# Kernel tuning notes

Hardware: AMD Instinct MI355X
Metric: run time of the kernel (lower is better)

## Reference

```python
import jax, jax.numpy as jnp
import numpy as np

N = 100000
E = 1600000
NFEAT = 128
NHID = 16
HEADS = 4
NCLASS = 40
NEG_SLOPE = 0.2
BN_EPS = 1e-5


def setup_inputs() -> dict:
    key = jax.random.key(0)
    ks = jax.random.split(key, 16)
    HC = NHID * HEADS  # 64
    x = jax.random.normal(ks[0], (N, NFEAT), dtype=jnp.float32)
    edge_index = jax.random.randint(ks[1], (2, E), 0, N, dtype=jnp.int64)
    def glorot(k, shape, fan_in):
        return jax.random.normal(k, shape, dtype=jnp.float32) * (1.0 / np.sqrt(fan_in))
    return {
        "x": x,
        "edge_index": edge_index,
        # layer 1: GATConv(NFEAT -> NHID, heads=HEADS, concat=True)
        "W1": glorot(ks[2], (NFEAT, HC), NFEAT),
        "att_src1": glorot(ks[3], (HEADS, NHID), NHID),
        "att_dst1": glorot(ks[4], (HEADS, NHID), NHID),
        "bias1": jnp.zeros((HC,), dtype=jnp.float32),
        # BatchNorm1d(HC), eval mode (running stats)
        "bn_gamma": jnp.ones((HC,), dtype=jnp.float32),
        "bn_beta": jnp.zeros((HC,), dtype=jnp.float32),
        "bn_mean": jax.random.normal(ks[5], (HC,), dtype=jnp.float32) * 0.1,
        "bn_var": jax.random.uniform(ks[6], (HC,), dtype=jnp.float32, minval=0.5, maxval=1.5),
        # layer 2: GATConv(HC -> NCLASS, heads=1, concat=False)
        "W2": glorot(ks[7], (HC, NCLASS), HC),
        "att_src2": glorot(ks[8], (1, NCLASS), NCLASS),
        "att_dst2": glorot(ks[9], (1, NCLASS), NCLASS),
        "bias2": jnp.zeros((NCLASS,), dtype=jnp.float32),
    }


def gat_conv(x, src, dst, W, att_src, att_dst, bias, concat):
    """PyG GATConv (eval; self-loops assumed already appended to src/dst)."""
    H, C = att_src.shape
    n = x.shape[0]
    h = (x @ W).reshape(n, H, C)                         # [N,H,C]
    a_s = (h * att_src[None]).sum(-1)                    # [N,H]
    a_d = (h * att_dst[None]).sum(-1)                    # [N,H]
    alpha = jax.nn.leaky_relu(a_s[src] + a_d[dst], NEG_SLOPE)  # [Et,H]
    # segment softmax over incoming edges of each destination node
    amax = jax.ops.segment_max(alpha, dst, num_segments=n)    # [N,H]
    ex = jnp.exp(alpha - amax[dst])
    denom = jax.ops.segment_sum(ex, dst, num_segments=n)
    coef = ex / denom[dst]                               # [Et,H]
    msg = h[src] * coef[:, :, None]                      # [Et,H,C]
    out = jax.ops.segment_sum(msg, dst, num_segments=n)  # [N,H,C]
    out = out.reshape(n, H * C) if concat else out.mean(axis=1)
    return out + bias


def reference(x, edge_index, W1, att_src1, att_dst1, bias1,
              bn_gamma, bn_beta, bn_mean, bn_var,
              W2, att_src2, att_dst2, bias2):
    n = x.shape[0]
    loops = jnp.arange(n, dtype=edge_index.dtype)
    src = jnp.concatenate([edge_index[0], loops])
    dst = jnp.concatenate([edge_index[1], loops])
    h = gat_conv(x, src, dst, W1, att_src1, att_dst1, bias1, concat=True)
    h = (h - bn_mean) * jax.lax.rsqrt(bn_var + BN_EPS) * bn_gamma + bn_beta
    h = jax.nn.relu(h)  # dropout is identity in eval
    out = gat_conv(h, src, dst, W2, att_src2, att_dst2, bias2, concat=False)
    return out
```

## Files before the change

### kernel.cpp

```cpp
#include <hip/hip_runtime.h>
#include <hip/hip_bf16.h>
#include <hip/hip_fp16.h>

#define NFEAT  128
#define HC     64
#define HEADS  4
#define NHID   16
#define NCLASS 40
#define NEG    0.2f
#define BN_EPS 1e-5f

#define BK_SH   9
#define CHUNK   8192
#define STAGE   12288

typedef _Float16 half8_t __attribute__((ext_vector_type(8)));
typedef _Float16 half4_t __attribute__((ext_vector_type(4)));
typedef float    f32x4_t __attribute__((ext_vector_type(4)));

__device__ __forceinline__ float leaky(float a) { return (a > 0.f) ? a : NEG * a; }

__global__ __launch_bounds__(256) void k_gemm1(
    const float* __restrict__ x, const float* __restrict__ W1,
    const float* __restrict__ att_s, const float* __restrict__ att_d,
    __half* __restrict__ h1, float* __restrict__ as1, float* __restrict__ ad1,
    int n)
{
    const int wave = threadIdx.x >> 6, lane = threadIdx.x & 63;
    const int quad = lane >> 4, l16 = lane & 15;

    half8_t bfrag[4][4];
    #pragma unroll
    for (int ks = 0; ks < 4; ++ks)
        #pragma unroll
        for (int ct = 0; ct < 4; ++ct)
            #pragma unroll
            for (int j = 0; j < 8; ++j)
                bfrag[ks][ct][j] =
                    (_Float16)W1[(ks * 32 + quad * 8 + j) * HC + ct * 16 + l16];

    float avs[4], avd[4];
    #pragma unroll
    for (int ct = 0; ct < 4; ++ct) {
        avs[ct] = att_s[ct * 16 + l16];
        avd[ct] = att_d[ct * 16 + l16];
    }

    const int nslab = (n + 15) >> 4;
    for (int slab = blockIdx.x * 4 + wave; slab < nslab; slab += gridDim.x * 4) {
        const int rowbase = slab * 16;
        const int arow = min(rowbase + l16, n - 1);
        const float* xp = x + (size_t)arow * NFEAT;

        f32x4_t acc[4] = {{0.f,0.f,0.f,0.f},{0.f,0.f,0.f,0.f},
                          {0.f,0.f,0.f,0.f},{0.f,0.f,0.f,0.f}};
        #pragma unroll
        for (int ks = 0; ks < 4; ++ks) {
            const float4 xa = *(const float4*)(xp + ks * 32 + quad * 8);
            const float4 xb = *(const float4*)(xp + ks * 32 + quad * 8 + 4);
            half8_t af;
            af[0] = (_Float16)xa.x; af[1] = (_Float16)xa.y;
            af[2] = (_Float16)xa.z; af[3] = (_Float16)xa.w;
            af[4] = (_Float16)xb.x; af[5] = (_Float16)xb.y;
            af[6] = (_Float16)xb.z; af[7] = (_Float16)xb.w;
            #pragma unroll
            for (int ct = 0; ct < 4; ++ct)
                acc[ct] = __builtin_amdgcn_mfma_f32_16x16x32_f16(
                    af, bfrag[ks][ct], acc[ct], 0, 0, 0);
        }

        #pragma unroll
        for (int reg = 0; reg < 4; ++reg) {
            const int row = rowbase + quad * 4 + reg;
            const bool valid = row < n;

            float4 ps, pd;
            ps.x = acc[0][reg] * avs[0]; pd.x = acc[0][reg] * avd[0];
            ps.y = acc[1][reg] * avs[1]; pd.y = acc[1][reg] * avd[1];
            ps.z = acc[2][reg] * avs[2]; pd.z = acc[2][reg] * avd[2];
            ps.w = acc[3][reg] * avs[3]; pd.w = acc[3][reg] * avd[3];
            #pragma unroll
            for (int off = 8; off >= 1; off >>= 1) {
                ps.x += __shfl_xor(ps.x, off, 64); pd.x += __shfl_xor(pd.x, off, 64);
                ps.y += __shfl_xor(ps.y, off, 64); pd.y += __shfl_xor(pd.y, off, 64);
                ps.z += __shfl_xor(ps.z, off, 64); pd.z += __shfl_xor(pd.z, off, 64);
                ps.w += __shfl_xor(ps.w, off, 64); pd.w += __shfl_xor(pd.w, off, 64);
            }
            if (valid) {
                #pragma unroll
                for (int ct = 0; ct < 4; ++ct)
                    h1[(size_t)row * HC + ct * 16 + l16] =
                        __float2half_rn(acc[ct][reg]);
                if (l16 == 0) {
                    *(float4*)(as1 + (size_t)row * HEADS) = ps;
                    *(float4*)(ad1 + (size_t)row * HEADS) = pd;
                }
            }
        }
    }
}

__global__ __launch_bounds__(512) void k_hist(
    const int* __restrict__ edst, int* __restrict__ hist, int E, int nbk)
{
    __shared__ int lh[256];
    const int w = blockIdx.x, t = threadIdx.x;
    for (int i = t; i < nbk; i += 512) lh[i] = 0;
    __syncthreads();
    const int lo = w * CHUNK, hi = min(E, lo + CHUNK);
    for (int e = lo + 4 * t; e < hi; e += 4 * 512) {
        const int4 d4 = *(const int4*)(edst + e);
        atomicAdd(&lh[d4.x >> BK_SH], 1);
        atomicAdd(&lh[d4.y >> BK_SH], 1);
        atomicAdd(&lh[d4.z >> BK_SH], 1);
        atomicAdd(&lh[d4.w >> BK_SH], 1);
    }
    __syncthreads();
    for (int i = t; i < nbk; i += 512) hist[(size_t)w * nbk + i] = lh[i];
}

__global__ __launch_bounds__(256) void k_colscan(
    int* __restrict__ hist, int* __restrict__ colsum, int nbk, int nw)
{
    __shared__ int wred[4];
    const int b = blockIdx.x, t = threadIdx.x;
    const int lane = t & 63, w = t >> 6;
    const int v = (t < nw) ? hist[(size_t)t * nbk + b] : 0;
    int sc = v;
    #pragma unroll
    for (int off = 1; off < 64; off <<= 1) {
        int u = __shfl_up(sc, off, 64);
        if (lane >= off) sc += u;
    }
    if (lane == 63) wred[w] = sc;
    __syncthreads();
    if (t == 0) { int a = 0; for (int i = 0; i < 4; ++i) { int xx = wred[i]; wred[i] = a; a += xx; } }
    __syncthreads();
    const int excl = sc - v + wred[w];
    if (t < nw) hist[(size_t)t * nbk + b] = excl;
    if (t == nw - 1) colsum[b] = excl + v;
}

__global__ __launch_bounds__(256) void k_bscan(
    const int* __restrict__ colsum, int* __restrict__ bstart, int nbk, int E)
{
    __shared__ int wred[4];
    const int t = threadIdx.x, lane = t & 63, w = t >> 6;
    const int v = (t < nbk) ? colsum[t] : 0;
    int sc = v;
    #pragma unroll
    for (int off = 1; off < 64; off <<= 1) {
        int u = __shfl_up(sc, off, 64);
        if (lane >= off) sc += u;
    }
    if (lane == 63) wred[w] = sc;
    __syncthreads();
    if (t == 0) { int a = 0; for (int i = 0; i < 4; ++i) { int xx = wred[i]; wred[i] = a; a += xx; } }
    __syncthreads();
    if (t < nbk) bstart[t] = sc - v + wred[w];
    if (t == 0) bstart[nbk] = E;
}

__global__ __launch_bounds__(512) void k_scatter(
    const int* __restrict__ esrc, const int* __restrict__ edst,
    const int* __restrict__ hist, const int* __restrict__ bstart,
    int2* __restrict__ pairs, int E, int nbk)
{
    __shared__ int cur[256];
    const int w = blockIdx.x, t = threadIdx.x;
    for (int i = t; i < nbk; i += 512)
        cur[i] = bstart[i] + hist[(size_t)w * nbk + i];
    __syncthreads();
    const int lo = w * CHUNK, hi = min(E, lo + CHUNK);
    for (int e = lo + 4 * t; e < hi; e += 4 * 512) {
        const int4 s4 = *(const int4*)(esrc + e);
        const int4 d4 = *(const int4*)(edst + e);
        int pos;
        pos = atomicAdd(&cur[d4.x >> BK_SH], 1); pairs[pos] = make_int2(s4.x, d4.x);
        pos = atomicAdd(&cur[d4.y >> BK_SH], 1); pairs[pos] = make_int2(s4.y, d4.y);
        pos = atomicAdd(&cur[d4.z >> BK_SH], 1); pairs[pos] = make_int2(s4.z, d4.z);
        pos = atomicAdd(&cur[d4.w >> BK_SH], 1); pairs[pos] = make_int2(s4.w, d4.w);
    }
}

__global__ __launch_bounds__(512) void k_build(
    const int2* __restrict__ pairs, const int* __restrict__ bstart,
    int* __restrict__ rowptr, int* __restrict__ csr, int n, int nbk)
{
    __shared__ int cnt[512];
    __shared__ int cur[512];
    __shared__ int stage[STAGE];
    __shared__ int wred[8];
    const int b = blockIdx.x, t = threadIdx.x;
    const int base = bstart[b], eend = bstart[b + 1], m = eend - base;
    const int n0 = b << BK_SH;
    const int nn = min(512, n - n0);

    cnt[t] = 0;
    __syncthreads();
    for (int e = base + t; e < eend; e += 512)
        atomicAdd(&cnt[pairs[e].y - n0], 1);
    __syncthreads();

    const int v = cnt[t];
    const int lane = t & 63, w = t >> 6;
    int sc = v;
    #pragma unroll
    for (int off = 1; off < 64; off <<= 1) {
        int u = __shfl_up(sc, off, 64);
        if (lane >= off) sc += u;
    }
    if (lane == 63) wred[w] = sc;
    __syncthreads();
    if (t == 0) { int a = 0; for (int i = 0; i < 8; ++i) { int xx = wred[i]; wred[i] = a; a += xx; } }
    __syncthreads();
    const int excl = sc - v + wred[w];
    cur[t] = excl;
    if (t < nn) rowptr[n0 + t] = base + excl + v;
    __syncthreads();

    for (int e = base + t; e < eend; e += 512) {
        const int2 p = pairs[e];
        const int loc = atomicAdd(&cur[p.y - n0], 1);
        if (loc < STAGE) stage[loc] = p.x;
        else             csr[base + loc] = p.x;
    }
    __syncthreads();
    const int lim = min(m, STAGE);
    for (int i = t; i < lim; i += 512) csr[base + i] = stage[i];
}

__global__ __launch_bounds__(256, 4) void k_agg1(
    const int* __restrict__ csr, const int* __restrict__ rowptr,
    const __half* __restrict__ h1, const float* __restrict__ as1,
    const float* __restrict__ ad1,
    const float* __restrict__ bias1, const float* __restrict__ gamma,
    const float* __restrict__ beta, const float* __restrict__ mean,
    const float* __restrict__ var,
    const float* __restrict__ W2, const float* __restrict__ ats2,
    const float* __restrict__ atd2,
    __half* __restrict__ g, float* __restrict__ as2o, float* __restrict__ ad2o,
    int n)
{
    __shared__ _Float16 sWh[NCLASS * HC];
    __shared__ float sh[16][68];
    __shared__ float sE[16][4][20];
    for (int i = threadIdx.x; i < NCLASS * HC; i += 256) sWh[i] = (_Float16)W2[i];
    __syncthreads();

    const int gi = threadIdx.x >> 4;
    const int q  = threadIdx.x & 15;
    const int myh = q >> 2;
    const unsigned nclamp = (unsigned)(n - 1);

    const float4 b1v = *(const float4*)(bias1 + 4 * q);
    const float4 gmv = *(const float4*)(gamma + 4 * q);
    const float4 vrv = *(const float4*)(var   + 4 * q);
    const float4 mnv = *(const float4*)(mean  + 4 * q);
    const float4 btv = *(const float4*)(beta  + 4 * q);
    float4 scv, shv;
    scv.x = gmv.x * rsqrtf(vrv.x + BN_EPS);
    scv.y = gmv.y * rsqrtf(vrv.y + BN_EPS);
    scv.z = gmv.z * rsqrtf(vrv.z + BN_EPS);
    scv.w = gmv.w * rsqrtf(vrv.w + BN_EPS);
    shv.x = btv.x - mnv.x * scv.x;
    shv.y = btv.y - mnv.y * scv.y;
    shv.z = btv.z - mnv.z * scv.z;
    shv.w = btv.w - mnv.w * scv.w;
    float4 at2 = {0.f, 0.f, 0.f, 0.f}, dt2 = {0.f, 0.f, 0.f, 0.f};
    if (q < 10) {
        at2 = *(const float4*)(ats2 + 4 * q);
        dt2 = *(const float4*)(atd2 + 4 * q);
    }

    for (int node0 = blockIdx.x * 16; node0 < n; node0 += gridDim.x * 16) {
        const int node = node0 + gi;
        if (node >= n) continue;

        const float4 adv = *(const float4*)(ad1 + node * HEADS);
        const float4 sv4 = *(const float4*)(as1 + node * HEADS);
        float4 eself;
        eself.x = __expf(leaky(sv4.x + adv.x));
        eself.y = __expf(leaky(sv4.y + adv.y));
        eself.z = __expf(leaky(sv4.z + adv.z));
        eself.w = __expf(leaky(sv4.w + adv.w));
        const float es = (myh == 0) ? eself.x : (myh == 1) ? eself.y
                       : (myh == 2) ? eself.z : eself.w;

        float4 acc;
        {
            const half4_t hv = *(const half4_t*)(h1 + (size_t)node * HC + 4 * q);
            acc.x = es * (float)hv[0]; acc.y = es * (float)hv[1];
            acc.z = es * (float)hv[2]; acc.w = es * (float)hv[3];
        }
        float4 dpart = {0.f, 0.f, 0.f, 0.f};

        const int start = (node == 0) ? 0 : rowptr[node - 1];
        const int end   = rowptr[node];

        for (int base = start; base < end; base += 16) {
            const int m = end - base;
            const int* cb = csr + base;

            const int myraw = cb[min(q, m - 1)];
            int idxs[16];
            #pragma unroll
            for (int e = 0; e < 16; ++e) idxs[e] = cb[e];

            half4_t wreg[16];
            #pragma unroll
            for (int e = 0; e < 16; ++e) {
                const unsigned off =
                    (min((unsigned)idxs[e], nclamp) << 7) + ((unsigned)q << 3);
                wreg[e] = *(const half4_t*)((const char*)h1 + off);
            }
            const float4 s4 =
                *(const float4*)(as1 + (size_t)min((unsigned)myraw, nclamp) * HEADS);
            __builtin_amdgcn_sched_barrier(0);

            const bool val = q < m;
            float4 ea;
            ea.x = val ? __expf(leaky(s4.x + adv.x)) : 0.f;
            ea.y = val ? __expf(leaky(s4.y + adv.y)) : 0.f;
            ea.z = val ? __expf(leaky(s4.z + adv.z)) : 0.f;
            ea.w = val ? __expf(leaky(s4.w + adv.w)) : 0.f;
            dpart.x += ea.x; dpart.y += ea.y;
            dpart.z += ea.z; dpart.w += ea.w;
            sE[gi][0][q] = ea.x;
            sE[gi][1][q] = ea.y;
            sE[gi][2][q] = ea.z;
            sE[gi][3][q] = ea.w;

            float eev[16];
            *(float4*)&eev[0]  = *(const float4*)&sE[gi][myh][0];
            *(float4*)&eev[4]  = *(const float4*)&sE[gi][myh][4];
            *(float4*)&eev[8]  = *(const float4*)&sE[gi][myh][8];
            *(float4*)&eev[12] = *(const float4*)&sE[gi][myh][12];

            #pragma unroll
            for (int e = 0; e < 16; ++e) {
                const float ee = eev[e];
                acc.x = fmaf((float)wreg[e][0], ee, acc.x);
                acc.y = fmaf((float)wreg[e][1], ee, acc.y);
                acc.z = fmaf((float)wreg[e][2], ee, acc.z);
                acc.w = fmaf((float)wreg[e][3], ee, acc.w);
            }
        }

        #pragma unroll
        for (int off = 8; off >= 1; off >>= 1) {
            dpart.x += __shfl_xor(dpart.x, off, 64);
            dpart.y += __shfl_xor(dpart.y, off, 64);
            dpart.z += __shfl_xor(dpart.z, off, 64);
            dpart.w += __shfl_xor(dpart.w, off, 64);
        }
        const float den = es + ((myh == 0) ? dpart.x : (myh == 1) ? dpart.y
                               : (myh == 2) ? dpart.z : dpart.w);
        const float rden = 1.f / den;

        float4 v;
        v.x = fmaxf(fmaf(acc.x * rden + b1v.x, scv.x, shv.x), 0.f);
        v.y = fmaxf(fmaf(acc.y * rden + b1v.y, scv.y, shv.y), 0.f);
        v.z = fmaxf(fmaf(acc.z * rden + b1v.z, scv.z, shv.z), 0.f);
        v.w = fmaxf(fmaf(acc.w * rden + b1v.w, scv.w, shv.w), 0.f);
        *(float4*)&sh[gi][4 * q] = v;

        float4 gacc = {0.f, 0.f, 0.f, 0.f};
        if (q < 10) {
            #pragma unroll 8
            for (int k = 0; k < HC; ++k) {
                const float hk = sh[gi][k];
                const half4_t wv = *(const half4_t*)&sWh[k * NCLASS + 4 * q];
                gacc.x = fmaf(hk, (float)wv[0], gacc.x);
                gacc.y = fmaf(hk, (float)wv[1], gacc.y);
                gacc.z = fmaf(hk, (float)wv[2], gacc.z);
                gacc.w = fmaf(hk, (float)wv[3], gacc.w);
            }
        }
        __half2 p0 = __float22half2_rn({gacc.x, gacc.y});
        __half2 p1 = __float22half2_rn({gacc.z, gacc.w});
        float2 packed; *(__half2*)&packed.x = p0; *(__half2*)&packed.y = p1;
        *(float2*)(g + (size_t)node * HC + 4 * q) = packed;

        float sv = gacc.x * at2.x + gacc.y * at2.y + gacc.z * at2.z + gacc.w * at2.w;
        float dv = gacc.x * dt2.x + gacc.y * dt2.y + gacc.z * dt2.z + gacc.w * dt2.w;
        #pragma unroll
        for (int off = 8; off >= 1; off >>= 1) {
            sv += __shfl_xor(sv, off, 64);
            dv += __shfl_xor(dv, off, 64);
        }
        if (q == 0) { as2o[node] = sv; ad2o[node] = dv; }
    }
}

__global__ __launch_bounds__(256, 4) void k_agg2(
    const int* __restrict__ csr, const int* __restrict__ rowptr,
    const __half* __restrict__ g, const float* __restrict__ as2,
    const float* __restrict__ ad2, const float* __restrict__ bias2,
    float* __restrict__ out, int n)
{
    __shared__ float sE[16][17];
    __shared__ int   sS[16][17];
    const int gi = threadIdx.x >> 4;
    const int q  = threadIdx.x & 15;

    float4 b2v = {0.f, 0.f, 0.f, 0.f};
    if (q < 10) b2v = *(const float4*)(bias2 + 4 * q);

    for (int node0 = blockIdx.x * 16; node0 < n; node0 += gridDim.x * 16) {
        const int node = node0 + gi;
        if (node >= n) continue;

        const float ad2d = ad2[node];
        const float eself = __expf(leaky(as2[node] + ad2d));

        float2 raws = *(const float2*)(g + (size_t)node * HC + 4 * q);
        const float2 s0v = __half22float2(*(__half2*)&raws.x);
        const float2 s1v = __half22float2(*(__half2*)&raws.y);
        float4 acc;
        acc.x = eself * s0v.x; acc.y = eself * s0v.y;
        acc.z = eself * s1v.x; acc.w = eself * s1v.y;
        float dpart = 0.f;

        const int start = (node == 0) ? 0 : rowptr[node - 1];
        const int end   = rowptr[node];

        if (start < end) {
            int ia = csr[min(start + q, end - 1)];
            for (int base = start; base < end; base += 16) {
                const int m = end - base;

                const float sca = as2[ia];
                const int ia_next = csr[min(base + 16 + q, end - 1)];

                sS[gi][q] = ia;

                int idxs[16];
                #pragma unroll
                for (int e = 0; e < 16; ++e) idxs[e] = sS[gi][e];

                float2 wreg[16];
                #pragma unroll
                for (int e = 0; e < 16; ++e)
                    wreg[e] = *(const float2*)(g + (size_t)idxs[e] * HC + 4 * q);
                __builtin_amdgcn_sched_barrier(0);

                const float ea = (q < m) ? __expf(leaky(sca + ad2d)) : 0.f;
                dpart += ea;
                sE[gi][q] = ea;

                #pragma unroll
                for (int e = 0; e < 16; ++e) {
                    const float ee = sE[gi][e];
                    const float2 a0 = __half22float2(*(const __half2*)&wreg[e].x);
                    const float2 a1 = __half22float2(*(const __half2*)&wreg[e].y);
                    acc.x = fmaf(ee, a0.x, acc.x); acc.y = fmaf(ee, a0.y, acc.y);
                    acc.z = fmaf(ee, a1.x, acc.z); acc.w = fmaf(ee, a1.y, acc.w);
                }
                ia = ia_next;
            }
        }

        #pragma unroll
        for (int off = 8; off >= 1; off >>= 1)
            dpart += __shfl_xor(dpart, off, 64);
        const float rden = 1.f / (dpart + eself);

        if (q < 10) {
            float4 r;
            r.x = acc.x * rden + b2v.x;
            r.y = acc.y * rden + b2v.y;
            r.z = acc.z * rden + b2v.z;
            r.w = acc.w * rden + b2v.w;
            *(float4*)(out + (size_t)node * NCLASS + 4 * q) = r;
        }
    }
}

extern "C" void kernel_launch(void* const* d_in, const int* in_sizes, int n_in,
                              void* d_out, int out_size, void* d_ws, size_t ws_size,
                              hipStream_t stream)
{
    const float* x    = (const float*)d_in[0];
    const int*   ei   = (const int*)  d_in[1];
    const float* W1   = (const float*)d_in[2];
    const float* as1w = (const float*)d_in[3];
    const float* ad1w = (const float*)d_in[4];
    const float* b1   = (const float*)d_in[5];
    const float* gm   = (const float*)d_in[6];
    const float* bt   = (const float*)d_in[7];
    const float* mn   = (const float*)d_in[8];
    const float* vr   = (const float*)d_in[9];
    const float* W2   = (const float*)d_in[10];
    const float* as2w = (const float*)d_in[11];
    const float* ad2w = (const float*)d_in[12];
    const float* b2   = (const float*)d_in[13];

    const int n = in_sizes[0] / NFEAT;
    const int E = in_sizes[1] / 2;
    const int* esrc = ei;
    const int* edst = ei + E;

    const int nbk = (n + 511) >> BK_SH;
    const int nw  = (E + CHUNK - 1) / CHUNK;

    float*  ws   = (float*)d_ws;
    __half* h1   = (__half*)ws;
    float*  a_s1 = ws   + (size_t)n * 32;
    float*  a_d1 = a_s1 + (size_t)n * 4;
    __half* gbuf = (__half*)(a_d1 + (size_t)n * 4);
    float*  a_s2 = a_d1 + (size_t)n * 4 + (size_t)n * 32;
    float*  a_d2 = a_s2 + n;
    int2*   pairs  = (int2*)(a_d2 + n);
    int*    csr    = (int*)(pairs + E);
    int*    rowptr = csr + E;
    int*    hist   = rowptr + n;
    int*    colsum = hist + (size_t)nw * nbk;
    int*    bstart = colsum + nbk;
    float*  outv = (float*)d_out;

    const int nblk1 = 2048;
    const int nblk2 = (n + 15) / 16;

    k_hist   <<<nw, 512, 0, stream>>>(edst, hist, E, nbk);
    k_colscan<<<nbk, 256, 0, stream>>>(hist, colsum, nbk, nw);
    k_bscan  <<<1, 256, 0, stream>>>(colsum, bstart, nbk, E);
    k_scatter<<<nw, 512, 0, stream>>>(esrc, edst, hist, bstart, pairs, E, nbk);
    k_build  <<<nbk, 512, 0, stream>>>(pairs, bstart, rowptr, csr, n, nbk);
    k_gemm1  <<<512, 256, 0, stream>>>(x, W1, as1w, ad1w, h1, a_s1, a_d1, n);
    k_agg1   <<<nblk1, 256, 0, stream>>>(csr, rowptr, h1, a_s1, a_d1,
                                         b1, gm, bt, mn, vr,
                                         W2, as2w, ad2w, gbuf, a_s2, a_d2, n);
    k_agg2   <<<nblk2, 256, 0, stream>>>(csr, rowptr, gbuf, a_s2, a_d2,
                                         b2, outv, n);
}
```

Before: 255.0 us.

## Split layer-2 projection out of agg1 into a separate MFMA GEMM kernel

Moves the per-node 64x40 W2 projection and the attention-logit dot products out of the first aggregation kernel, where each node did a scalar FMA loop over LDS, into a new kernel built on 16x16x32 f16 MFMA. agg1 now writes the post-BN/ReLU hidden features as fp16 into a buffer that reuses the pairs workspace, and k_gemm2 reads them back to produce g and the layer-2 attention scalars. This drops LDS traffic and scalar work from agg1 and may raise its occupancy. In exchange it adds a kernel launch and an extra write and read of the 100000x64 fp16 intermediate.

```diff
diff --git a/kernel.cpp b/kernel.cpp
--- a/kernel.cpp
+++ b/kernel.cpp
@@ -100,6 +100,79 @@
     }
 }
 
+__global__ __launch_bounds__(256) void k_gemm2(
+    const __half* __restrict__ h2, const float* __restrict__ W2,
+    const float* __restrict__ ats2, const float* __restrict__ atd2,
+    __half* __restrict__ g, float* __restrict__ as2, float* __restrict__ ad2,
+    int n)
+{
+    const int wave = threadIdx.x >> 6, lane = threadIdx.x & 63;
+    const int quad = lane >> 4, l16 = lane & 15;
+
+    half8_t bfrag[2][3];
+    #pragma unroll
+    for (int ks = 0; ks < 2; ++ks)
+        #pragma unroll
+        for (int ct = 0; ct < 3; ++ct)
+            #pragma unroll
+            for (int j = 0; j < 8; ++j) {
+                const int c = ct * 16 + l16;
+                bfrag[ks][ct][j] = (c < NCLASS)
+                    ? (_Float16)W2[(ks * 32 + quad * 8 + j) * NCLASS + c]
+                    : (_Float16)0.f;
+            }
+
+    float avs[3], avd[3];
+    #pragma unroll
+    for (int ct = 0; ct < 3; ++ct) {
+        const int c = ct * 16 + l16;
+        avs[ct] = (c < NCLASS) ? ats2[c] : 0.f;
+        avd[ct] = (c < NCLASS) ? atd2[c] : 0.f;
+    }
+
+    const int nslab = (n + 15) >> 4;
+    for (int slab = blockIdx.x * 4 + wave; slab < nslab; slab += gridDim.x * 4) {
+        const int rowbase = slab * 16;
+        const int arow = min(rowbase + l16, n - 1);
+        const __half* hp = h2 + (size_t)arow * HC;
+
+        f32x4_t acc[3] = {{0.f,0.f,0.f,0.f},{0.f,0.f,0.f,0.f},
+                          {0.f,0.f,0.f,0.f}};
+        #pragma unroll
+        for (int ks = 0; ks < 2; ++ks) {
+            const half8_t af = *(const half8_t*)(hp + ks * 32 + quad * 8);
+            #pragma unroll
+            for (int ct = 0; ct < 3; ++ct)
+                acc[ct] = __builtin_amdgcn_mfma_f32_16x16x32_f16(
+                    af, bfrag[ks][ct], acc[ct], 0, 0, 0);
+        }
+
+        #pragma unroll
+        for (int reg = 0; reg < 4; ++reg) {
+            const int row = rowbase + quad * 4 + reg;
+            const bool valid = row < n;
+
+            float sv = acc[0][reg] * avs[0] + acc[1][reg] * avs[1]
+                     + acc[2][reg] * avs[2];
+            float dv = acc[0][reg] * avd[0] + acc[1][reg] * avd[1]
+                     + acc[2][reg] * avd[2];
+            #pragma unroll
+            for (int off = 8; off >= 1; off >>= 1) {
+                sv += __shfl_xor(sv, off, 64);
+                dv += __shfl_xor(dv, off, 64);
+            }
+            if (valid) {
+                #pragma unroll
+                for (int ct = 0; ct < 3; ++ct)
+                    g[(size_t)row * HC + ct * 16 + l16] =
+                        __float2half_rn(acc[ct][reg]);
+                g[(size_t)row * HC + 48 + l16] = __float2half_rn(0.f);
+                if (l16 == 0) { as2[row] = sv; ad2[row] = dv; }
+            }
+        }
+    }
+}
+
 __global__ __launch_bounds__(512) void k_hist(
     const int* __restrict__ edst, int* __restrict__ hist, int E, int nbk)
 {
@@ -237,16 +310,9 @@
     const float* __restrict__ bias1, const float* __restrict__ gamma,
     const float* __restrict__ beta, const float* __restrict__ mean,
     const float* __restrict__ var,
-    const float* __restrict__ W2, const float* __restrict__ ats2,
-    const float* __restrict__ atd2,
-    __half* __restrict__ g, float* __restrict__ as2o, float* __restrict__ ad2o,
-    int n)
-{
-    __shared__ _Float16 sWh[NCLASS * HC];
-    __shared__ float sh[16][68];
+    __half* __restrict__ h2, int n)
+{
     __shared__ float sE[16][4][20];
-    for (int i = threadIdx.x; i < NCLASS * HC; i += 256) sWh[i] = (_Float16)W2[i];
-    __syncthreads();
 
     const int gi = threadIdx.x >> 4;
     const int q  = threadIdx.x & 15;
@@ -267,11 +333,6 @@
     shv.y = btv.y - mnv.y * scv.y;
     shv.z = btv.z - mnv.z * scv.z;
     shv.w = btv.w - mnv.w * scv.w;
-    float4 at2 = {0.f, 0.f, 0.f, 0.f}, dt2 = {0.f, 0.f, 0.f, 0.f};
-    if (q < 10) {
-        at2 = *(const float4*)(ats2 + 4 * q);
-        dt2 = *(const float4*)(atd2 + 4 * q);
-    }
 
     for (int node0 = blockIdx.x * 16; node0 < n; node0 += gridDim.x * 16) {
         const int node = node0 + gi;
@@ -363,33 +424,11 @@
         v.y = fmaxf(fmaf(acc.y * rden + b1v.y, scv.y, shv.y), 0.f);
         v.z = fmaxf(fmaf(acc.z * rden + b1v.z, scv.z, shv.z), 0.f);
         v.w = fmaxf(fmaf(acc.w * rden + b1v.w, scv.w, shv.w), 0.f);
-        *(float4*)&sh[gi][4 * q] = v;
-
-        float4 gacc = {0.f, 0.f, 0.f, 0.f};
-        if (q < 10) {
-            #pragma unroll 8
-            for (int k = 0; k < HC; ++k) {
-                const float hk = sh[gi][k];
-                const half4_t wv = *(const half4_t*)&sWh[k * NCLASS + 4 * q];
-                gacc.x = fmaf(hk, (float)wv[0], gacc.x);
-                gacc.y = fmaf(hk, (float)wv[1], gacc.y);
-                gacc.z = fmaf(hk, (float)wv[2], gacc.z);
-                gacc.w = fmaf(hk, (float)wv[3], gacc.w);
-            }
-        }
-        __half2 p0 = __float22half2_rn({gacc.x, gacc.y});
-        __half2 p1 = __float22half2_rn({gacc.z, gacc.w});
-        float2 packed; *(__half2*)&packed.x = p0; *(__half2*)&packed.y = p1;
-        *(float2*)(g + (size_t)node * HC + 4 * q) = packed;
-
-        float sv = gacc.x * at2.x + gacc.y * at2.y + gacc.z * at2.z + gacc.w * at2.w;
-        float dv = gacc.x * dt2.x + gacc.y * dt2.y + gacc.z * dt2.z + gacc.w * dt2.w;
-        #pragma unroll
-        for (int off = 8; off >= 1; off >>= 1) {
-            sv += __shfl_xor(sv, off, 64);
-            dv += __shfl_xor(dv, off, 64);
-        }
-        if (q == 0) { as2o[node] = sv; ad2o[node] = dv; }
+
+        half4_t hv2;
+        hv2[0] = (_Float16)v.x; hv2[1] = (_Float16)v.y;
+        hv2[2] = (_Float16)v.z; hv2[3] = (_Float16)v.w;
+        *(half4_t*)(h2 + (size_t)node * HC + 4 * q) = hv2;
     }
 }
 
@@ -519,6 +558,8 @@
     int*    bstart = colsum + nbk;
     float*  outv = (float*)d_out;
 
+    __half* h2buf = (__half*)pairs;
+
     const int nblk1 = 2048;
     const int nblk2 = (n + 15) / 16;
 
@@ -529,8 +570,9 @@
     k_build  <<<nbk, 512, 0, stream>>>(pairs, bstart, rowptr, csr, n, nbk);
     k_gemm1  <<<512, 256, 0, stream>>>(x, W1, as1w, ad1w, h1, a_s1, a_d1, n);
     k_agg1   <<<nblk1, 256, 0, stream>>>(csr, rowptr, h1, a_s1, a_d1,
-                                         b1, gm, bt, mn, vr,
-                                         W2, as2w, ad2w, gbuf, a_s2, a_d2, n);
+                                         b1, gm, bt, mn, vr, h2buf, n);
+    k_gemm2  <<<512, 256, 0, stream>>>(h2buf, W2, as2w, ad2w,
+                                       gbuf, a_s2, a_d2, n);
     k_agg2   <<<nblk2, 256, 0, stream>>>(csr, rowptr, gbuf, a_s2, a_d2,
                                          b2, outv, n);
 }
```

After: 250.3 us (median of 2 runs). Within noise of the previous version (-1.8%).
